# Kernel optimization log

Hardware: AMD Instinct MI355X
Metric: run time of the kernel (lower is better)

Reference implementation:

```python
import jax, jax.numpy as jnp
import numpy as np

EPS = 1e-5          # nn.LayerNorm default eps
THRESH = 0.4        # min_entity_score
K = 20              # max_entities_per_text
NUM_TYPES = 8       # len(EntityType) (not in source; fixed constant)


def _mlp(x, w1, b1, g, be, w2, b2):
    """Linear -> LayerNorm -> GELU(exact) -> (Dropout=eval identity) -> Linear."""
    h = x @ w1 + b1
    mu = h.mean(-1, keepdims=True)
    var = ((h - mu) ** 2).mean(-1, keepdims=True)
    h = (h - mu) * jax.lax.rsqrt(var + EPS) * g + be
    h = jax.nn.gelu(h, approximate=False)
    return h @ w2 + b2


def setup_inputs() -> dict:
    key = jax.random.key(0)
    ks = jax.random.split(key, 10)
    B, S, D, H, T = 8, 4096, 1024, 256, NUM_TYPES

    def lin(k, i, o):
        s = 1.0 / np.sqrt(i)
        return jax.random.uniform(k, (i, o), jnp.float32, -s, s)

    return {
        "hidden_states": jax.random.normal(ks[0], (B, S, D), jnp.float32),
        "attention_mask": jax.random.randint(ks[1], (B, S), 0, 2).astype(jnp.int32),
        # entity_scorer params
        "sc_w1": lin(ks[2], D, H), "sc_b1": jnp.zeros((H,), jnp.float32),
        "sc_g": jnp.ones((H,), jnp.float32), "sc_be": jnp.zeros((H,), jnp.float32),
        "sc_w2": lin(ks[3], H, 1), "sc_b2": jnp.zeros((1,), jnp.float32),
        # span_enhancer params
        "en_w1": lin(ks[4], D, H), "en_b1": jnp.zeros((H,), jnp.float32),
        "en_g": jnp.ones((H,), jnp.float32), "en_be": jnp.zeros((H,), jnp.float32),
        "en_w2": lin(ks[5], H, D), "en_b2": jnp.zeros((D,), jnp.float32),
        # type_classifier params
        "ty_w1": lin(ks[6], D, H), "ty_b1": jnp.zeros((H,), jnp.float32),
        "ty_g": jnp.ones((H,), jnp.float32), "ty_be": jnp.zeros((H,), jnp.float32),
        "ty_w2": lin(ks[7], H, T), "ty_b2": jnp.zeros((T,), jnp.float32),
    }


def reference(hidden_states, attention_mask,
              sc_w1, sc_b1, sc_g, sc_be, sc_w2, sc_b2,
              en_w1, en_b1, en_g, en_be, en_w2, en_b2,
              ty_w1, ty_b1, ty_g, ty_be, ty_w2, ty_b2):
    B, S, D = hidden_states.shape
    # per-token entity scores [B, S]
    scores = jax.nn.sigmoid(_mlp(hidden_states, sc_w1, sc_b1, sc_g, sc_be, sc_w2, sc_b2))[..., 0]
    scores = scores * attention_mask.astype(scores.dtype)
    # parallel run-length encoding of spans (replaces serial python loop):
    # a token is inside a span iff score >= thresh and unmasked; spans break on
    # below-threshold or masked tokens, exactly as the serial RLE does.
    above = (scores >= THRESH) & (attention_mask > 0)
    prev = jnp.pad(above[:, :-1], ((0, 0), (1, 0)))
    start = above & ~prev
    sid = jnp.clip(jnp.cumsum(start.astype(jnp.int32), axis=1) - 1, 0)  # span label per token
    seg = (sid + jnp.arange(B, dtype=jnp.int32)[:, None] * S).reshape(-1)
    w = above.astype(scores.dtype)
    nseg = B * S
    span_len = jax.ops.segment_sum(w.reshape(-1), seg, num_segments=nseg).reshape(B, S)
    span_sum = jax.ops.segment_sum((scores * w).reshape(-1), seg, num_segments=nseg).reshape(B, S)
    rep_sum = jax.ops.segment_sum((hidden_states * w[..., None]).reshape(B * S, D), seg,
                                  num_segments=nseg).reshape(B, S, D)
    denom = jnp.maximum(span_len, 1.0)
    avg = span_sum / denom                      # mean token score per span
    valid = (span_len > 0) & (avg >= THRESH)    # avg-score threshold from original
    sel = jnp.where(valid, avg, -1.0)
    # keep at most K highest-scoring spans per batch row (matches global sort + per-batch cap)
    top_vals, top_idx = jax.lax.top_k(sel, K)   # [B, K]
    valid_k = (top_vals >= THRESH).astype(scores.dtype)
    reps = jnp.take_along_axis(rep_sum, top_idx[..., None], axis=1)
    lens = jnp.take_along_axis(denom, top_idx, axis=1)
    reps = reps / lens[..., None] * valid_k[..., None]      # span mean-pooled hidden states
    enhanced = _mlp(reps, en_w1, en_b1, en_g, en_be, en_w2, en_b2) * valid_k[..., None]
    type_logits = _mlp(enhanced, ty_w1, ty_b1, ty_g, ty_be, ty_w2, ty_b2)
    type_probs = jax.nn.softmax(type_logits, axis=-1)
    entity_types = jnp.argmax(type_logits, axis=-1)
    entity_scores = top_vals * valid_k
    return scores, enhanced, type_logits, entity_scores, type_probs, entity_types, valid_k
```

## Files before the change

### kernel.cpp

```cpp
#include <hip/hip_runtime.h>
#include <hip/hip_bf16.h>

#define S_LEN 4096
#define BATCH 8
#define DMODEL 1024
#define HDIM 256
#define NTYPES 8
#define KMAX 20
#define NSLOT (BATCH*KMAX)
#define THRESH 0.4f
#define LN_EPS 1e-5f
#define RSQRT2 0.70710678118654752f

#define O_SCORES 0
#define O_ENH    32768
#define O_TLOG   196608
#define O_ESC    197888
#define O_TPROB  198048
#define O_TYPE   199328
#define O_VALIDK 199488

#define WS_SCORES   0
#define WS_SPSTART  32768
#define WS_SPLEN    49152
#define WS_SPAVG    65536
#define WS_NSP      81920
#define WS_SELSTART 81936
#define WS_SELLEN   82096
#define WS_SELAVG   82256
#define WS_SELVALID 82416
#define WS_IMG      82576

typedef _Float16 f16x2 __attribute__((ext_vector_type(2)));
typedef _Float16 f16x8 __attribute__((ext_vector_type(8)));
typedef float f32x16 __attribute__((ext_vector_type(16)));

#define APAD 40

__device__ __forceinline__ float gelu_exact(float v) {
    return 0.5f * v * (1.0f + erff(v * RSQRT2));
}

__global__ __launch_bounds__(256) void k_prep(
    const float* __restrict__ W1, _Float16* __restrict__ IMG)
{
    const int c = blockIdx.x;
    const int n = threadIdx.x;
    f16x8 hv[2], lv[2];
#pragma unroll
    for (int j = 0; j < 2; j++)
#pragma unroll
        for (int e = 0; e < 8; e++) {
            float w = W1[(size_t)(c * 16 + j * 8 + e) * HDIM + n];
            _Float16 h = (_Float16)w;
            hv[j][e] = h;
            lv[j][e] = (_Float16)(w - (float)h);
        }
    const int off = c * 8192 + n * 16;
    *(f16x8*)&IMG[off] = hv[0];
    *(f16x8*)&IMG[off + 8] = hv[1];
    *(f16x8*)&IMG[off + 4096] = lv[0];
    *(f16x8*)&IMG[off + 4096 + 8] = lv[1];
}

__global__ __launch_bounds__(512, 4) void k_score9(
    const float* __restrict__ X, const _Float16* __restrict__ IMG,
    const float* __restrict__ B1, const float* __restrict__ G,
    const float* __restrict__ BE, const float* __restrict__ W2,
    const float* __restrict__ B2, const int* __restrict__ MASK,
    float* __restrict__ scf, float* __restrict__ out)
{
    union SM {
        _Float16 A[2][2][64 * APAD];
        struct { float part2[64 * 5]; float mul[64]; float rsl[64]; } e;
    };
    __shared__ SM sm;

    const int tid = threadIdx.x;
    const int lane = tid & 63, wid = tid >> 6;
    const int lr = lane & 31, lh = lane >> 5;
    const int wm = (wid & 1) * 32;
    const int wn = (wid >> 1) * 64;
    const int wnid = wid >> 1;
    const int tok0 = blockIdx.x * 64;

    const int xrow = tid >> 3, xk = (tid & 7) * 2;
    const float* xbase = X + (size_t)(tok0 + xrow) * DMODEL + xk;
    const int awoff = xrow * APAD + xk;
    const int aroff = (wm + lr) * APAD + lh * 8;
    const int bo0 = (wn + lr) * 16 + lh * 8;
    const int bo1 = (wn + 32 + lr) * 16 + lh * 8;

    f32x16 acc0 = (f32x16)0.0f, acc1 = (f32x16)0.0f;

    float2 x0 = *(const float2*)xbase;
    f16x8 bh0c = *(const f16x8*)&IMG[bo0];
    f16x8 bh1c = *(const f16x8*)&IMG[bo1];
    f16x8 bl0c = *(const f16x8*)&IMG[4096 + bo0];
    f16x8 bl1c = *(const f16x8*)&IMG[4096 + bo1];
    {
        _Float16 h0 = (_Float16)x0.x, h1 = (_Float16)x0.y;
        f16x2 hh = {h0, h1};
        f16x2 ll = {(_Float16)(x0.x - (float)h0), (_Float16)(x0.y - (float)h1)};
        *(f16x2*)&sm.A[0][0][awoff] = hh;
        *(f16x2*)&sm.A[0][1][awoff] = ll;
    }
    float2 xnext = *(const float2*)(xbase + 16);
    f16x8 bh0n = *(const f16x8*)&IMG[8192 + bo0];
    f16x8 bh1n = *(const f16x8*)&IMG[8192 + bo1];
    f16x8 bl0n = *(const f16x8*)&IMG[8192 + 4096 + bo0];
    f16x8 bl1n = *(const f16x8*)&IMG[8192 + 4096 + bo1];
    asm volatile("s_waitcnt lgkmcnt(0)" ::: "memory");
    __builtin_amdgcn_s_barrier();
    __builtin_amdgcn_sched_barrier(0);

    int cur = 0;
#pragma unroll
    for (int c = 0; c < 64; ++c) {
        const int cf = (c + 2) & 63;
        float2 xfut = *(const float2*)(xbase + cf * 16);
        const _Float16* ib = IMG + cf * 8192;
        f16x8 fbh0 = *(const f16x8*)&ib[bo0];
        f16x8 fbh1 = *(const f16x8*)&ib[bo1];
        f16x8 fbl0 = *(const f16x8*)&ib[4096 + bo0];
        f16x8 fbl1 = *(const f16x8*)&ib[4096 + bo1];

        f16x8 fah = *(const f16x8*)&sm.A[cur][0][aroff];
        f16x8 fal = *(const f16x8*)&sm.A[cur][1][aroff];

        acc0 = __builtin_amdgcn_mfma_f32_32x32x16_f16(fah, bh0c, acc0, 0, 0, 0);
        acc0 = __builtin_amdgcn_mfma_f32_32x32x16_f16(fal, bh0c, acc0, 0, 0, 0);
        acc0 = __builtin_amdgcn_mfma_f32_32x32x16_f16(fah, bl0c, acc0, 0, 0, 0);
        acc1 = __builtin_amdgcn_mfma_f32_32x32x16_f16(fah, bh1c, acc1, 0, 0, 0);
        acc1 = __builtin_amdgcn_mfma_f32_32x32x16_f16(fal, bh1c, acc1, 0, 0, 0);
        acc1 = __builtin_amdgcn_mfma_f32_32x32x16_f16(fah, bl1c, acc1, 0, 0, 0);

        {
            _Float16 h0 = (_Float16)xnext.x, h1 = (_Float16)xnext.y;
            f16x2 hh = {h0, h1};
            f16x2 ll = {(_Float16)(xnext.x - (float)h0), (_Float16)(xnext.y - (float)h1)};
            *(f16x2*)&sm.A[cur ^ 1][0][awoff] = hh;
            *(f16x2*)&sm.A[cur ^ 1][1][awoff] = ll;
        }
        asm volatile("s_waitcnt lgkmcnt(0)" ::: "memory");
        __builtin_amdgcn_s_barrier();
        __builtin_amdgcn_sched_barrier(0);

        bh0c = bh0n; bh1c = bh1n; bl0c = bl0n; bl1c = bl1n;
        bh0n = fbh0; bh1n = fbh1; bl0n = fbl0; bl1n = fbl1;
        xnext = xfut;
        cur ^= 1;
    }

    __syncthreads();

    float bcol[2], gcol[2], becol[2], wcol[2];
#pragma unroll
    for (int ni = 0; ni < 2; ni++) {
        int colg = wn + ni * 32 + lr;
        bcol[ni] = B1[colg];
        gcol[ni] = G[colg];
        becol[ni] = BE[colg];
        wcol[ni] = W2[colg];
    }
#pragma unroll
    for (int r = 0; r < 16; r++) { acc0[r] += bcol[0]; acc1[r] += bcol[1]; }

#pragma unroll
    for (int r = 0; r < 16; r++) {
        float p = acc0[r] + acc1[r];
        p += __shfl_xor(p, 1);  p += __shfl_xor(p, 2);
        p += __shfl_xor(p, 4);  p += __shfl_xor(p, 8);
        p += __shfl_xor(p, 16);
        int row = wm + (r & 3) + 8 * (r >> 2) + 4 * lh;
        if (lr == 0) sm.e.part2[row * 5 + wnid] = p;
    }
    __syncthreads();
    if (tid < 64)
        sm.e.mul[tid] = (sm.e.part2[tid * 5] + sm.e.part2[tid * 5 + 1] +
                         sm.e.part2[tid * 5 + 2] + sm.e.part2[tid * 5 + 3]) * (1.0f / 256.0f);
    __syncthreads();
#pragma unroll
    for (int r = 0; r < 16; r++) {
        int row = wm + (r & 3) + 8 * (r >> 2) + 4 * lh;
        float m = sm.e.mul[row];
        float d0 = acc0[r] - m, d1 = acc1[r] - m;
        float p = d0 * d0 + d1 * d1;
        p += __shfl_xor(p, 1);  p += __shfl_xor(p, 2);
        p += __shfl_xor(p, 4);  p += __shfl_xor(p, 8);
        p += __shfl_xor(p, 16);
        if (lr == 0) sm.e.part2[row * 5 + wnid] = p;
    }
    __syncthreads();
    if (tid < 64)
        sm.e.rsl[tid] = rsqrtf((sm.e.part2[tid * 5] + sm.e.part2[tid * 5 + 1] +
                                sm.e.part2[tid * 5 + 2] + sm.e.part2[tid * 5 + 3]) * (1.0f / 256.0f) + LN_EPS);
    __syncthreads();
#pragma unroll
    for (int r = 0; r < 16; r++) {
        int row = wm + (r & 3) + 8 * (r >> 2) + 4 * lh;
        float m = sm.e.mul[row];
        float rv = sm.e.rsl[row];
        float v0 = (acc0[r] - m) * rv * gcol[0] + becol[0];
        float v1 = (acc1[r] - m) * rv * gcol[1] + becol[1];
        float p = gelu_exact(v0) * wcol[0] + gelu_exact(v1) * wcol[1];
        p += __shfl_xor(p, 1);  p += __shfl_xor(p, 2);
        p += __shfl_xor(p, 4);  p += __shfl_xor(p, 8);
        p += __shfl_xor(p, 16);
        if (lr == 0) sm.e.part2[row * 5 + wnid] = p;
    }
    __syncthreads();
    if (tid < 64) {
        float s = sm.e.part2[tid * 5] + sm.e.part2[tid * 5 + 1] +
                  sm.e.part2[tid * 5 + 2] + sm.e.part2[tid * 5 + 3];
        float logit = s + B2[0];
        float sc = 1.0f / (1.0f + expf(-logit));
        int t = tok0 + tid;
        sc *= (float)MASK[t];
        scf[t] = sc;
        out[O_SCORES + t] = sc;
    }
}

__global__ __launch_bounds__(1024) void k_spans(
    const float* __restrict__ scf, int* __restrict__ spstart,
    int* __restrict__ splen, float* __restrict__ spavg, int* __restrict__ nsp,
    int* __restrict__ selstart, int* __restrict__ sellen,
    float* __restrict__ selavg, float* __restrict__ selvalid,
    float* __restrict__ out)
{
    const int r = blockIdx.x, tid = threadIdx.x;
    __shared__ float sc[S_LEN];
    __shared__ unsigned char ab[S_LEN];
    __shared__ int scn[1024];
    __shared__ float avgl[2048];
    __shared__ float rv[16];
    __shared__ int ri[16];

    float4 v = ((const float4*)(scf + (size_t)r * S_LEN))[tid];
    const int s0 = tid * 4;
    sc[s0 + 0] = v.x; sc[s0 + 1] = v.y; sc[s0 + 2] = v.z; sc[s0 + 3] = v.w;
    ab[s0 + 0] = (v.x >= THRESH);
    ab[s0 + 1] = (v.y >= THRESH);
    ab[s0 + 2] = (v.z >= THRESH);
    ab[s0 + 3] = (v.w >= THRESH);
    __syncthreads();

    bool st[4];
    int cnt = 0;
#pragma unroll
    for (int i = 0; i < 4; i++) {
        bool a = ab[s0 + i] != 0;
        bool p = (s0 + i == 0) ? false : (ab[s0 + i - 1] != 0);
        st[i] = a && !p;
        cnt += st[i] ? 1 : 0;
    }
    scn[tid] = cnt;
    __syncthreads();
    for (int off = 1; off < 1024; off <<= 1) {
        int mine = scn[tid];
        int add = (tid >= off) ? scn[tid - off] : 0;
        __syncthreads();
        scn[tid] = mine + add;
        __syncthreads();
    }
    const int total = scn[1023];
    int j = scn[tid] - cnt;
    for (int i = 0; i < 4; i++) {
        if (st[i]) {
            int s = s0 + i;
            float sum = 0.0f;
            int len = 0;
            int e = s;
            while (e < S_LEN && ab[e]) { sum += sc[e]; len++; e++; }
            float avg = sum / (float)len;
            spstart[r * 2048 + j] = s;
            splen[r * 2048 + j] = len;
            spavg[r * 2048 + j] = avg;
            avgl[j] = avg;
            j++;
        }
    }
    if (tid == 0) nsp[r] = total;
    __syncthreads();

    for (int k = 0; k < KMAX; k++) {
        float bv = -3.0e38f;
        int bi = 0x7FFFFFFF;
        for (int q = tid; q < total; q += 1024) {
            float a = avgl[q];
            if (a > bv) { bv = a; bi = q; }
        }
#pragma unroll
        for (int m = 1; m < 64; m <<= 1) {
            float ov = __shfl_xor(bv, m);
            int oi = __shfl_xor(bi, m);
            if (ov > bv || (ov == bv && oi < bi)) { bv = ov; bi = oi; }
        }
        if ((tid & 63) == 0) { rv[tid >> 6] = bv; ri[tid >> 6] = bi; }
        __syncthreads();
        if (tid < 64) {
            float v2 = (tid < 16) ? rv[tid] : -3.0e38f;
            int i2 = (tid < 16) ? ri[tid] : 0x7FFFFFFF;
#pragma unroll
            for (int m = 1; m < 16; m <<= 1) {
                float ov = __shfl_xor(v2, m);
                int oi = __shfl_xor(i2, m);
                if (ov > v2 || (ov == v2 && oi < i2)) { v2 = ov; i2 = oi; }
            }
            if (tid == 0) {
                int slot = r * KMAX + k;
                if (k < total) {
                    avgl[i2] = -3.0e38f;
                    int ln = splen[r * 2048 + i2];
                    float vd = (v2 >= THRESH && ln > 0) ? 1.0f : 0.0f;
                    selstart[slot] = spstart[r * 2048 + i2];
                    sellen[slot] = ln;
                    selavg[slot] = v2;
                    selvalid[slot] = vd;
                    out[O_ESC + slot] = v2 * vd;
                    out[O_VALIDK + slot] = vd;
                } else {
                    selstart[slot] = -1;
                    sellen[slot] = 0;
                    selavg[slot] = -1.0f;
                    selvalid[slot] = 0.0f;
                    out[O_ESC + slot] = 0.0f;
                    out[O_VALIDK + slot] = 0.0f;
                }
            }
        }
        __syncthreads();
    }
}

__global__ __launch_bounds__(1024) void k_tail2(
    const float* __restrict__ X, const int* __restrict__ selstart,
    const int* __restrict__ sellen, const float* __restrict__ selvalid,
    const float* __restrict__ en_w1, const float* __restrict__ en_b1,
    const float* __restrict__ en_g, const float* __restrict__ en_be,
    const float* __restrict__ en_w2, const float* __restrict__ en_b2,
    const float* __restrict__ ty_w1, const float* __restrict__ ty_b1,
    const float* __restrict__ ty_g, const float* __restrict__ ty_be,
    const float* __restrict__ ty_w2, const float* __restrict__ ty_b2,
    float* __restrict__ out)
{
    const int slot = blockIdx.x, tid = threadIdx.x;
    __shared__ float xr[DMODEL];
    __shared__ float ps[DMODEL];
    __shared__ float g1[HDIM];
    __shared__ float red[8];
    __shared__ float lgp[4 * NTYPES];
    __shared__ float lg[NTYPES];

    const int r = slot / KMAX;
    const int s0 = selstart[slot], ln = sellen[slot];
    const float vd = selvalid[slot];
    const int j = tid & 255, p = tid >> 8;

    {
        float a = 0.0f;
        if (s0 >= 0) {
            const float* base = X + ((size_t)r * S_LEN + s0) * DMODEL + tid;
#pragma unroll 4
            for (int t = 0; t < ln; t++) a += base[(size_t)t * DMODEL];
        }
        const float dn = (ln > 0) ? (float)ln : 1.0f;
        xr[tid] = a / dn * vd;
    }
    __syncthreads();

    {
        float acc = 0.0f;
        const float* wp = en_w1 + (size_t)(p * 256) * HDIM + j;
        const float* xp = xr + p * 256;
#pragma unroll 16
        for (int k = 0; k < 256; k++) acc += xp[k] * wp[(size_t)k * HDIM];
        ps[tid] = acc;
    }
    __syncthreads();
    float h = 0.0f, mu = 0.0f;
    if (tid < 256) {
        h = ps[tid] + ps[256 + tid] + ps[512 + tid] + ps[768 + tid] + en_b1[tid];
        float s = h;
#pragma unroll
        for (int m = 1; m < 64; m <<= 1) s += __shfl_xor(s, m);
        if ((tid & 63) == 0) red[tid >> 6] = s;
    }
    __syncthreads();
    if (tid < 256) {
        mu = (red[0] + red[1] + red[2] + red[3]) * (1.0f / 256.0f);
        float d = h - mu;
        float s = d * d;
#pragma unroll
        for (int m = 1; m < 64; m <<= 1) s += __shfl_xor(s, m);
        if ((tid & 63) == 0) red[4 + (tid >> 6)] = s;
    }
    __syncthreads();
    if (tid < 256) {
        float var = (red[4] + red[5] + red[6] + red[7]) * (1.0f / 256.0f);
        float v = (h - mu) * rsqrtf(var + LN_EPS) * en_g[tid] + en_be[tid];
        g1[tid] = gelu_exact(v);
    }
    __syncthreads();

    {
        float acc = en_b2[tid];
        const float* wp = en_w2 + tid;
#pragma unroll 16
        for (int k = 0; k < 256; k++) acc += g1[k] * wp[(size_t)k * DMODEL];
        acc *= vd;
        out[O_ENH + (size_t)slot * DMODEL + tid] = acc;
        xr[tid] = acc;
    }
    __syncthreads();

    {
        float acc = 0.0f;
        const float* wp = ty_w1 + (size_t)(p * 256) * HDIM + j;
        const float* xp = xr + p * 256;
#pragma unroll 16
        for (int k = 0; k < 256; k++) acc += xp[k] * wp[(size_t)k * HDIM];
        ps[tid] = acc;
    }
    __syncthreads();
    h = 0.0f; mu = 0.0f;
    if (tid < 256) {
        h = ps[tid] + ps[256 + tid] + ps[512 + tid] + ps[768 + tid] + ty_b1[tid];
        float s = h;
#pragma unroll
        for (int m = 1; m < 64; m <<= 1) s += __shfl_xor(s, m);
        if ((tid & 63) == 0) red[tid >> 6] = s;
    }
    __syncthreads();
    if (tid < 256) {
        mu = (red[0] + red[1] + red[2] + red[3]) * (1.0f / 256.0f);
        float d = h - mu;
        float s = d * d;
#pragma unroll
        for (int m = 1; m < 64; m <<= 1) s += __shfl_xor(s, m);
        if ((tid & 63) == 0) red[4 + (tid >> 6)] = s;
    }
    __syncthreads();
    if (tid < 256) {
        float var = (red[4] + red[5] + red[6] + red[7]) * (1.0f / 256.0f);
        float v = (h - mu) * rsqrtf(var + LN_EPS) * ty_g[tid] + ty_be[tid];
        g1[tid] = gelu_exact(v);
    }
    __syncthreads();

    if (tid < 256) {
        float gv = g1[tid];
        float4 w0 = *(const float4*)&ty_w2[tid * NTYPES];
        float4 w1v = *(const float4*)&ty_w2[tid * NTYPES + 4];
        float pj[8] = {gv * w0.x, gv * w0.y, gv * w0.z, gv * w0.w,
                       gv * w1v.x, gv * w1v.y, gv * w1v.z, gv * w1v.w};
#pragma unroll
        for (int q = 0; q < 8; q++) {
            float s = pj[q];
#pragma unroll
            for (int m = 1; m < 64; m <<= 1) s += __shfl_xor(s, m);
            pj[q] = s;
        }
        if ((tid & 63) == 0) {
#pragma unroll
            for (int q = 0; q < 8; q++) lgp[(tid >> 6) * NTYPES + q] = pj[q];
        }
    }
    __syncthreads();
    if (tid < NTYPES) {
        float la = ty_b2[tid] + lgp[tid] + lgp[NTYPES + tid] +
                   lgp[2 * NTYPES + tid] + lgp[3 * NTYPES + tid];
        lg[tid] = la;
        out[O_TLOG + slot * NTYPES + tid] = la;
    }
    __syncthreads();
    if (tid == 0) {
        float mx = lg[0];
        int am = 0;
        for (int t = 1; t < NTYPES; t++)
            if (lg[t] > mx) { mx = lg[t]; am = t; }
        float ex[NTYPES], ssum = 0.0f;
        for (int t = 0; t < NTYPES; t++) { ex[t] = expf(lg[t] - mx); ssum += ex[t]; }
        for (int t = 0; t < NTYPES; t++)
            out[O_TPROB + slot * NTYPES + t] = ex[t] / ssum;
        out[O_TYPE + slot] = (float)am;
    }
}

extern "C" void kernel_launch(void* const* d_in, const int* in_sizes, int n_in,
                              void* d_out, int out_size, void* d_ws, size_t ws_size,
                              hipStream_t stream) {
    const float* X = (const float*)d_in[0];
    const int* MASK = (const int*)d_in[1];
    const float* sc_w1 = (const float*)d_in[2];
    const float* sc_b1 = (const float*)d_in[3];
    const float* sc_g  = (const float*)d_in[4];
    const float* sc_be = (const float*)d_in[5];
    const float* sc_w2 = (const float*)d_in[6];
    const float* sc_b2 = (const float*)d_in[7];
    const float* en_w1 = (const float*)d_in[8];
    const float* en_b1 = (const float*)d_in[9];
    const float* en_g  = (const float*)d_in[10];
    const float* en_be = (const float*)d_in[11];
    const float* en_w2 = (const float*)d_in[12];
    const float* en_b2 = (const float*)d_in[13];
    const float* ty_w1 = (const float*)d_in[14];
    const float* ty_b1 = (const float*)d_in[15];
    const float* ty_g  = (const float*)d_in[16];
    const float* ty_be = (const float*)d_in[17];
    const float* ty_w2 = (const float*)d_in[18];
    const float* ty_b2 = (const float*)d_in[19];

    float* out = (float*)d_out;
    float* wsf = (float*)d_ws;
    int* wsi = (int*)d_ws;
    _Float16* img = (_Float16*)(wsf + WS_IMG);

    k_prep<<<64, 256, 0, stream>>>(sc_w1, img);
    k_score9<<<(BATCH * S_LEN) / 64, 512, 0, stream>>>(
        X, img, sc_b1, sc_g, sc_be, sc_w2, sc_b2, MASK, wsf + WS_SCORES, out);
    k_spans<<<BATCH, 1024, 0, stream>>>(
        wsf + WS_SCORES, wsi + WS_SPSTART, wsi + WS_SPLEN, wsf + WS_SPAVG,
        wsi + WS_NSP, wsi + WS_SELSTART, wsi + WS_SELLEN, wsf + WS_SELAVG,
        wsf + WS_SELVALID, out);
    k_tail2<<<NSLOT, 1024, 0, stream>>>(
        X, wsi + WS_SELSTART, wsi + WS_SELLEN, wsf + WS_SELVALID,
        en_w1, en_b1, en_g, en_be, en_w2, en_b2,
        ty_w1, ty_b1, ty_g, ty_be, ty_w2, ty_b2, out);
}
```

Baseline: 150.3 us.

## Rewrite span extraction as single-wavefront kernel using ballot-based compaction

Replaces the 1024-thread span kernel, which used a block-wide Hillis-Steele scan with many __syncthreads and a two-level top-k reduction, with a 64-thread single-wavefront kernel. Span starts are compacted with __ballot/popcount over 64 sequential groups, span metadata is kept in shared memory instead of global workspace, and top-k uses only wavefront shuffles. This removes barrier and global-write overhead but serializes the work into far fewer threads, so per-row latency depends on the serial loops.

```diff
diff --git a/kernel.cpp b/kernel.cpp
--- a/kernel.cpp
+++ b/kernel.cpp
@@ -21,13 +21,8 @@
 #define O_VALIDK 199488
 
 #define WS_SCORES   0
-#define WS_SPSTART  32768
-#define WS_SPLEN    49152
-#define WS_SPAVG    65536
-#define WS_NSP      81920
 #define WS_SELSTART 81936
 #define WS_SELLEN   82096
-#define WS_SELAVG   82256
 #define WS_SELVALID 82416
 #define WS_IMG      82576
 
@@ -222,72 +217,56 @@
     }
 }
 
-__global__ __launch_bounds__(1024) void k_spans(
-    const float* __restrict__ scf, int* __restrict__ spstart,
-    int* __restrict__ splen, float* __restrict__ spavg, int* __restrict__ nsp,
-    int* __restrict__ selstart, int* __restrict__ sellen,
-    float* __restrict__ selavg, float* __restrict__ selvalid,
+__global__ __launch_bounds__(64) void k_spans64(
+    const float* __restrict__ scf, int* __restrict__ selstart,
+    int* __restrict__ sellen, float* __restrict__ selvalid,
     float* __restrict__ out)
 {
-    const int r = blockIdx.x, tid = threadIdx.x;
+    const int r = blockIdx.x, lane = threadIdx.x;
     __shared__ float sc[S_LEN];
     __shared__ unsigned char ab[S_LEN];
-    __shared__ int scn[1024];
     __shared__ float avgl[2048];
-    __shared__ float rv[16];
-    __shared__ int ri[16];
-
-    float4 v = ((const float4*)(scf + (size_t)r * S_LEN))[tid];
-    const int s0 = tid * 4;
-    sc[s0 + 0] = v.x; sc[s0 + 1] = v.y; sc[s0 + 2] = v.z; sc[s0 + 3] = v.w;
-    ab[s0 + 0] = (v.x >= THRESH);
-    ab[s0 + 1] = (v.y >= THRESH);
-    ab[s0 + 2] = (v.z >= THRESH);
-    ab[s0 + 3] = (v.w >= THRESH);
-    __syncthreads();
-
-    bool st[4];
-    int cnt = 0;
-#pragma unroll
-    for (int i = 0; i < 4; i++) {
-        bool a = ab[s0 + i] != 0;
-        bool p = (s0 + i == 0) ? false : (ab[s0 + i - 1] != 0);
-        st[i] = a && !p;
-        cnt += st[i] ? 1 : 0;
-    }
-    scn[tid] = cnt;
-    __syncthreads();
-    for (int off = 1; off < 1024; off <<= 1) {
-        int mine = scn[tid];
-        int add = (tid >= off) ? scn[tid - off] : 0;
-        __syncthreads();
-        scn[tid] = mine + add;
-        __syncthreads();
-    }
-    const int total = scn[1023];
-    int j = scn[tid] - cnt;
-    for (int i = 0; i < 4; i++) {
-        if (st[i]) {
-            int s = s0 + i;
+    __shared__ int lst[2048];
+    __shared__ int lln[2048];
+
+    const float* row = scf + (size_t)r * S_LEN;
+#pragma unroll
+    for (int i = 0; i < 16; i++) {
+        float4 v = ((const float4*)row)[lane + i * 64];
+        const int s0 = (lane + i * 64) * 4;
+        *(float4*)&sc[s0] = v;
+        uchar4 abv = {(unsigned char)(v.x >= THRESH), (unsigned char)(v.y >= THRESH),
+                      (unsigned char)(v.z >= THRESH), (unsigned char)(v.w >= THRESH)};
+        *(uchar4*)&ab[s0] = abv;
+    }
+    __syncthreads();
+
+    int gbase = 0;
+    for (int g = 0; g < 64; g++) {
+        const int t = g * 64 + lane;
+        const bool a = ab[t] != 0;
+        const bool p = (t == 0) ? false : (ab[t - 1] != 0);
+        const bool st = a && !p;
+        const unsigned long long mask = __ballot(st);
+        if (st) {
+            int j = gbase + __popcll(mask & ((1ull << lane) - 1ull));
             float sum = 0.0f;
             int len = 0;
-            int e = s;
+            int e = t;
             while (e < S_LEN && ab[e]) { sum += sc[e]; len++; e++; }
-            float avg = sum / (float)len;
-            spstart[r * 2048 + j] = s;
-            splen[r * 2048 + j] = len;
-            spavg[r * 2048 + j] = avg;
-            avgl[j] = avg;
-            j++;
-        }
-    }
-    if (tid == 0) nsp[r] = total;
+            avgl[j] = sum / (float)len;
+            lst[j] = t;
+            lln[j] = len;
+        }
+        gbase += __popcll(mask);
+    }
+    const int total = gbase;
     __syncthreads();
 
     for (int k = 0; k < KMAX; k++) {
         float bv = -3.0e38f;
         int bi = 0x7FFFFFFF;
-        for (int q = tid; q < total; q += 1024) {
+        for (int q = lane; q < total; q += 64) {
             float a = avgl[q];
             if (a > bv) { bv = a; bi = q; }
         }
@@ -297,37 +276,23 @@
             int oi = __shfl_xor(bi, m);
             if (ov > bv || (ov == bv && oi < bi)) { bv = ov; bi = oi; }
         }
-        if ((tid & 63) == 0) { rv[tid >> 6] = bv; ri[tid >> 6] = bi; }
-        __syncthreads();
-        if (tid < 64) {
-            float v2 = (tid < 16) ? rv[tid] : -3.0e38f;
-            int i2 = (tid < 16) ? ri[tid] : 0x7FFFFFFF;
-#pragma unroll
-            for (int m = 1; m < 16; m <<= 1) {
-                float ov = __shfl_xor(v2, m);
-                int oi = __shfl_xor(i2, m);
-                if (ov > v2 || (ov == v2 && oi < i2)) { v2 = ov; i2 = oi; }
-            }
-            if (tid == 0) {
-                int slot = r * KMAX + k;
-                if (k < total) {
-                    avgl[i2] = -3.0e38f;
-                    int ln = splen[r * 2048 + i2];
-                    float vd = (v2 >= THRESH && ln > 0) ? 1.0f : 0.0f;
-                    selstart[slot] = spstart[r * 2048 + i2];
-                    sellen[slot] = ln;
-                    selavg[slot] = v2;
-                    selvalid[slot] = vd;
-                    out[O_ESC + slot] = v2 * vd;
-                    out[O_VALIDK + slot] = vd;
-                } else {
-                    selstart[slot] = -1;
-                    sellen[slot] = 0;
-                    selavg[slot] = -1.0f;
-                    selvalid[slot] = 0.0f;
-                    out[O_ESC + slot] = 0.0f;
-                    out[O_VALIDK + slot] = 0.0f;
-                }
+        if (lane == 0) {
+            const int slot = r * KMAX + k;
+            if (k < total) {
+                avgl[bi] = -3.0e38f;
+                const int ln = lln[bi];
+                const float vd = (bv >= THRESH && ln > 0) ? 1.0f : 0.0f;
+                selstart[slot] = lst[bi];
+                sellen[slot] = ln;
+                selvalid[slot] = vd;
+                out[O_ESC + slot] = bv * vd;
+                out[O_VALIDK + slot] = vd;
+            } else {
+                selstart[slot] = -1;
+                sellen[slot] = 0;
+                selvalid[slot] = 0.0f;
+                out[O_ESC + slot] = 0.0f;
+                out[O_VALIDK + slot] = 0.0f;
             }
         }
         __syncthreads();
@@ -520,9 +485,8 @@
     k_prep<<<64, 256, 0, stream>>>(sc_w1, img);
     k_score9<<<(BATCH * S_LEN) / 64, 512, 0, stream>>>(
         X, img, sc_b1, sc_g, sc_be, sc_w2, sc_b2, MASK, wsf + WS_SCORES, out);
-    k_spans<<<BATCH, 1024, 0, stream>>>(
-        wsf + WS_SCORES, wsi + WS_SPSTART, wsi + WS_SPLEN, wsf + WS_SPAVG,
-        wsi + WS_NSP, wsi + WS_SELSTART, wsi + WS_SELLEN, wsf + WS_SELAVG,
+    k_spans64<<<BATCH, 64, 0, stream>>>(
+        wsf + WS_SCORES, wsi + WS_SELSTART, wsi + WS_SELLEN,
         wsf + WS_SELVALID, out);
     k_tail2<<<NSLOT, 1024, 0, stream>>>(
         X, wsi + WS_SELSTART, wsi + WS_SELLEN, wsf + WS_SELVALID,
```

After: 187.3 us. 1.25x slower.

## Load X fragments directly into registers, removing LDS staging and per-chunk barriers

Applied to the files above, without the earlier changes.

The scoring GEMM no longer stages split-fp16 X tiles through a double-buffered shared-memory buffer with a barrier per chunk. Each wave now loads its own MFMA A-fragment from global memory as float4 pairs and splits it into hi/lo halves in registers. This removes LDS writes and reads and 64 block barriers. In exchange, X rows are fetched redundantly by the four column-waves, relying on the cache, and the explicit software prefetch of future chunks is gone.

```diff
diff --git a/kernel.cpp b/kernel.cpp
--- a/kernel.cpp
+++ b/kernel.cpp
@@ -31,11 +31,8 @@
 #define WS_SELVALID 82416
 #define WS_IMG      82576
 
-typedef _Float16 f16x2 __attribute__((ext_vector_type(2)));
 typedef _Float16 f16x8 __attribute__((ext_vector_type(8)));
 typedef float f32x16 __attribute__((ext_vector_type(16)));
-
-#define APAD 40
 
 __device__ __forceinline__ float gelu_exact(float v) {
     return 0.5f * v * (1.0f + erff(v * RSQRT2));
@@ -63,18 +60,16 @@
     *(f16x8*)&IMG[off + 4096 + 8] = lv[1];
 }
 
-__global__ __launch_bounds__(512, 4) void k_score9(
+__global__ __launch_bounds__(512, 4) void k_score10(
     const float* __restrict__ X, const _Float16* __restrict__ IMG,
     const float* __restrict__ B1, const float* __restrict__ G,
     const float* __restrict__ BE, const float* __restrict__ W2,
     const float* __restrict__ B2, const int* __restrict__ MASK,
     float* __restrict__ scf, float* __restrict__ out)
 {
-    union SM {
-        _Float16 A[2][2][64 * APAD];
-        struct { float part2[64 * 5]; float mul[64]; float rsl[64]; } e;
-    };
-    __shared__ SM sm;
+    __shared__ float part2[64 * 5];
+    __shared__ float mul[64];
+    __shared__ float rsl[64];
 
     const int tid = threadIdx.x;
     const int lane = tid & 63, wid = tid >> 6;
@@ -84,75 +79,38 @@
     const int wnid = wid >> 1;
     const int tok0 = blockIdx.x * 64;
 
-    const int xrow = tid >> 3, xk = (tid & 7) * 2;
-    const float* xbase = X + (size_t)(tok0 + xrow) * DMODEL + xk;
-    const int awoff = xrow * APAD + xk;
-    const int aroff = (wm + lr) * APAD + lh * 8;
+    const float* xfr = X + (size_t)(tok0 + wm + lr) * DMODEL + lh * 8;
     const int bo0 = (wn + lr) * 16 + lh * 8;
     const int bo1 = (wn + 32 + lr) * 16 + lh * 8;
 
     f32x16 acc0 = (f32x16)0.0f, acc1 = (f32x16)0.0f;
 
-    float2 x0 = *(const float2*)xbase;
-    f16x8 bh0c = *(const f16x8*)&IMG[bo0];
-    f16x8 bh1c = *(const f16x8*)&IMG[bo1];
-    f16x8 bl0c = *(const f16x8*)&IMG[4096 + bo0];
-    f16x8 bl1c = *(const f16x8*)&IMG[4096 + bo1];
-    {
-        _Float16 h0 = (_Float16)x0.x, h1 = (_Float16)x0.y;
-        f16x2 hh = {h0, h1};
-        f16x2 ll = {(_Float16)(x0.x - (float)h0), (_Float16)(x0.y - (float)h1)};
-        *(f16x2*)&sm.A[0][0][awoff] = hh;
-        *(f16x2*)&sm.A[0][1][awoff] = ll;
-    }
-    float2 xnext = *(const float2*)(xbase + 16);
-    f16x8 bh0n = *(const f16x8*)&IMG[8192 + bo0];
-    f16x8 bh1n = *(const f16x8*)&IMG[8192 + bo1];
-    f16x8 bl0n = *(const f16x8*)&IMG[8192 + 4096 + bo0];
-    f16x8 bl1n = *(const f16x8*)&IMG[8192 + 4096 + bo1];
-    asm volatile("s_waitcnt lgkmcnt(0)" ::: "memory");
-    __builtin_amdgcn_s_barrier();
-    __builtin_amdgcn_sched_barrier(0);
-
-    int cur = 0;
 #pragma unroll
     for (int c = 0; c < 64; ++c) {
-        const int cf = (c + 2) & 63;
-        float2 xfut = *(const float2*)(xbase + cf * 16);
-        const _Float16* ib = IMG + cf * 8192;
-        f16x8 fbh0 = *(const f16x8*)&ib[bo0];
-        f16x8 fbh1 = *(const f16x8*)&ib[bo1];
-        f16x8 fbl0 = *(const f16x8*)&ib[4096 + bo0];
-        f16x8 fbl1 = *(const f16x8*)&ib[4096 + bo1];
-
-        f16x8 fah = *(const f16x8*)&sm.A[cur][0][aroff];
-        f16x8 fal = *(const f16x8*)&sm.A[cur][1][aroff];
-
-        acc0 = __builtin_amdgcn_mfma_f32_32x32x16_f16(fah, bh0c, acc0, 0, 0, 0);
-        acc0 = __builtin_amdgcn_mfma_f32_32x32x16_f16(fal, bh0c, acc0, 0, 0, 0);
-        acc0 = __builtin_amdgcn_mfma_f32_32x32x16_f16(fah, bl0c, acc0, 0, 0, 0);
-        acc1 = __builtin_amdgcn_mfma_f32_32x32x16_f16(fah, bh1c, acc1, 0, 0, 0);
-        acc1 = __builtin_amdgcn_mfma_f32_32x32x16_f16(fal, bh1c, acc1, 0, 0, 0);
-        acc1 = __builtin_amdgcn_mfma_f32_32x32x16_f16(fah, bl1c, acc1, 0, 0, 0);
-
-        {
-            _Float16 h0 = (_Float16)xnext.x, h1 = (_Float16)xnext.y;
-            f16x2 hh = {h0, h1};
-            f16x2 ll = {(_Float16)(xnext.x - (float)h0), (_Float16)(xnext.y - (float)h1)};
-            *(f16x2*)&sm.A[cur ^ 1][0][awoff] = hh;
-            *(f16x2*)&sm.A[cur ^ 1][1][awoff] = ll;
-        }
-        asm volatile("s_waitcnt lgkmcnt(0)" ::: "memory");
-        __builtin_amdgcn_s_barrier();
-        __builtin_amdgcn_sched_barrier(0);
-
-        bh0c = bh0n; bh1c = bh1n; bl0c = bl0n; bl1c = bl1n;
-        bh0n = fbh0; bh1n = fbh1; bl0n = fbl0; bl1n = fbl1;
-        xnext = xfut;
-        cur ^= 1;
-    }
-
-    __syncthreads();
+        float4 xa = *(const float4*)(xfr + c * 16);
+        float4 xb = *(const float4*)(xfr + c * 16 + 4);
+        const _Float16* ib = IMG + (size_t)c * 8192;
+        f16x8 bh0 = *(const f16x8*)&ib[bo0];
+        f16x8 bh1 = *(const f16x8*)&ib[bo1];
+        f16x8 bl0 = *(const f16x8*)&ib[4096 + bo0];
+        f16x8 bl1 = *(const f16x8*)&ib[4096 + bo1];
+
+        float xv[8] = {xa.x, xa.y, xa.z, xa.w, xb.x, xb.y, xb.z, xb.w};
+        f16x8 ah, al;
+#pragma unroll
+        for (int e = 0; e < 8; e++) {
+            _Float16 h = (_Float16)xv[e];
+            ah[e] = h;
+            al[e] = (_Float16)(xv[e] - (float)h);
+        }
+
+        acc0 = __builtin_amdgcn_mfma_f32_32x32x16_f16(ah, bh0, acc0, 0, 0, 0);
+        acc0 = __builtin_amdgcn_mfma_f32_32x32x16_f16(al, bh0, acc0, 0, 0, 0);
+        acc0 = __builtin_amdgcn_mfma_f32_32x32x16_f16(ah, bl0, acc0, 0, 0, 0);
+        acc1 = __builtin_amdgcn_mfma_f32_32x32x16_f16(ah, bh1, acc1, 0, 0, 0);
+        acc1 = __builtin_amdgcn_mfma_f32_32x32x16_f16(al, bh1, acc1, 0, 0, 0);
+        acc1 = __builtin_amdgcn_mfma_f32_32x32x16_f16(ah, bl1, acc1, 0, 0, 0);
+    }
 
     float bcol[2], gcol[2], becol[2], wcol[2];
 #pragma unroll
@@ -173,46 +131,46 @@
         p += __shfl_xor(p, 4);  p += __shfl_xor(p, 8);
         p += __shfl_xor(p, 16);
         int row = wm + (r & 3) + 8 * (r >> 2) + 4 * lh;
-        if (lr == 0) sm.e.part2[row * 5 + wnid] = p;
+        if (lr == 0) part2[row * 5 + wnid] = p;
     }
     __syncthreads();
     if (tid < 64)
-        sm.e.mul[tid] = (sm.e.part2[tid * 5] + sm.e.part2[tid * 5 + 1] +
-                         sm.e.part2[tid * 5 + 2] + sm.e.part2[tid * 5 + 3]) * (1.0f / 256.0f);
+        mul[tid] = (part2[tid * 5] + part2[tid * 5 + 1] +
+                    part2[tid * 5 + 2] + part2[tid * 5 + 3]) * (1.0f / 256.0f);
     __syncthreads();
 #pragma unroll
     for (int r = 0; r < 16; r++) {
         int row = wm + (r & 3) + 8 * (r >> 2) + 4 * lh;
-        float m = sm.e.mul[row];
+        float m = mul[row];
         float d0 = acc0[r] - m, d1 = acc1[r] - m;
         float p = d0 * d0 + d1 * d1;
         p += __shfl_xor(p, 1);  p += __shfl_xor(p, 2);
         p += __shfl_xor(p, 4);  p += __shfl_xor(p, 8);
         p += __shfl_xor(p, 16);
-        if (lr == 0) sm.e.part2[row * 5 + wnid] = p;
+        if (lr == 0) part2[row * 5 + wnid] = p;
     }
     __syncthreads();
     if (tid < 64)
-        sm.e.rsl[tid] = rsqrtf((sm.e.part2[tid * 5] + sm.e.part2[tid * 5 + 1] +
-                                sm.e.part2[tid * 5 + 2] + sm.e.part2[tid * 5 + 3]) * (1.0f / 256.0f) + LN_EPS);
+        rsl[tid] = rsqrtf((part2[tid * 5] + part2[tid * 5 + 1] +
+                           part2[tid * 5 + 2] + part2[tid * 5 + 3]) * (1.0f / 256.0f) + LN_EPS);
     __syncthreads();
 #pragma unroll
     for (int r = 0; r < 16; r++) {
         int row = wm + (r & 3) + 8 * (r >> 2) + 4 * lh;
-        float m = sm.e.mul[row];
-        float rv = sm.e.rsl[row];
+        float m = mul[row];
+        float rv = rsl[row];
         float v0 = (acc0[r] - m) * rv * gcol[0] + becol[0];
         float v1 = (acc1[r] - m) * rv * gcol[1] + becol[1];
         float p = gelu_exact(v0) * wcol[0] + gelu_exact(v1) * wcol[1];
         p += __shfl_xor(p, 1);  p += __shfl_xor(p, 2);
         p += __shfl_xor(p, 4);  p += __shfl_xor(p, 8);
         p += __shfl_xor(p, 16);
-        if (lr == 0) sm.e.part2[row * 5 + wnid] = p;
+        if (lr == 0) part2[row * 5 + wnid] = p;
     }
     __syncthreads();
     if (tid < 64) {
-        float s = sm.e.part2[tid * 5] + sm.e.part2[tid * 5 + 1] +
-                  sm.e.part2[tid * 5 + 2] + sm.e.part2[tid * 5 + 3];
+        float s = part2[tid * 5] + part2[tid * 5 + 1] +
+                  part2[tid * 5 + 2] + part2[tid * 5 + 3];
         float logit = s + B2[0];
         float sc = 1.0f / (1.0f + expf(-logit));
         int t = tok0 + tid;
@@ -518,7 +476,7 @@
     _Float16* img = (_Float16*)(wsf + WS_IMG);
 
     k_prep<<<64, 256, 0, stream>>>(sc_w1, img);
-    k_score9<<<(BATCH * S_LEN) / 64, 512, 0, stream>>>(
+    k_score10<<<(BATCH * S_LEN) / 64, 512, 0, stream>>>(
         X, img, sc_b1, sc_g, sc_be, sc_w2, sc_b2, MASK, wsf + WS_SCORES, out);
     k_spans<<<BATCH, 1024, 0, stream>>>(
         wsf + WS_SCORES, wsi + WS_SPSTART, wsi + WS_SPLEN, wsf + WS_SPAVG,
```

New measurement: 194.4 us. 1.29x slower.
